# Performance work log

Hardware: AMD Instinct MI355X
Metric: run time of the kernel (lower is better)

Reference implementation:

```python
import jax, jax.numpy as jnp
import numpy as np
from jax import lax

NFEATS = 128
NMODES = 2
KH = KW = 3


def _conv_lstm_step(h, c, inp, W, b):
    """Standard ConvLSTMCell: conv over [inp, h] -> 4 gates -> c/h update.
    inp: (B, Cin, H, W); h, c: (B, nfeats, H, W); W: (4*nfeats, Cin+nfeats, 3, 3)."""
    z = lax.conv_general_dilated(
        jnp.concatenate([inp, h], axis=1), W,
        window_strides=(1, 1), padding='SAME',
        dimension_numbers=('NCHW', 'OIHW', 'NCHW'))
    z = z + b[None, :, None, None]
    i, f, o, g = jnp.split(z, 4, axis=1)
    c_next = jax.nn.sigmoid(f) * c + jax.nn.sigmoid(i) * jnp.tanh(g)
    h_next = jax.nn.sigmoid(o) * jnp.tanh(c_next)
    return h_next, c_next


def setup_inputs() -> dict:
    key = jax.random.key(0)
    ks = jax.random.split(key, 8)
    B, T, H, Wsp = 4, 8, 32, 32
    x1 = jax.random.normal(ks[0], (B, T, NFEATS, H, Wsp), dtype=jnp.float32)
    x2 = jax.random.normal(ks[1], (B, T, NFEATS, H, Wsp), dtype=jnp.float32)
    s = 0.02
    W1 = jax.random.normal(ks[2], (4 * NFEATS, NMODES * NFEATS + NFEATS, KH, KW), dtype=jnp.float32) * s
    b1 = jnp.zeros((4 * NFEATS,), dtype=jnp.float32)
    W2 = jax.random.normal(ks[3], (4 * NFEATS, 2 * NFEATS, KH, KW), dtype=jnp.float32) * s
    b2 = jnp.zeros((4 * NFEATS,), dtype=jnp.float32)
    W3 = jax.random.normal(ks[4], (4 * NFEATS, 2 * NFEATS, KH, KW), dtype=jnp.float32) * s
    b3 = jnp.zeros((4 * NFEATS,), dtype=jnp.float32)
    return {"x1": x1, "x2": x2, "W1": W1, "b1": b1, "W2": W2, "b2": b2, "W3": W3, "b3": b3}


def reference(x1, x2, W1, b1, W2, b2, W3, b3):
    # cat modalities on channel dim: (B, T, nmodes*nfeats, H, W)
    x = jnp.concatenate([x1, x2], axis=2)
    B, T, C, H, Wsp = x.shape
    zero = jnp.zeros((B, NFEATS, H, Wsp), dtype=x.dtype)
    carry0 = (zero, zero, zero, zero, zero, zero)  # h1,c1,h2,c2,h3,c3
    xs = jnp.moveaxis(x, 1, 0)  # (T, B, C, H, W)

    def step(carry, xt):
        h1, c1, h2, c2, h3, c3 = carry
        h1, c1 = _conv_lstm_step(h1, c1, xt, W1, b1)
        h2, c2 = _conv_lstm_step(h2, c2, h1, W2, b2)
        h3, c3 = _conv_lstm_step(h3, c3, h2, W3, b3)
        return (h1, c1, h2, c2, h3, c3), None

    (h1, c1, h2, c2, h3, c3), _ = lax.scan(step, carry0, xs)
    return h3
```

## Files before the change

### kernel.cpp

```cpp
#include <hip/hip_runtime.h>
#include <hip/hip_bf16.h>

typedef unsigned short u16;
typedef __attribute__((ext_vector_type(8))) short short8;
typedef __attribute__((ext_vector_type(4))) short short4v;
typedef __attribute__((ext_vector_type(4))) float floatx4;

__device__ __forceinline__ u16 f2bf(float x) {
  unsigned u = __float_as_uint(x);
  u += 0x7fffu + ((u >> 16) & 1u);
  return (u16)(u >> 16);
}
__device__ __forceinline__ float bf2f(u16 u) {
  return __uint_as_float(((unsigned)u) << 16);
}
__device__ __forceinline__ float sigm(float x) {
  return 1.0f / (1.0f + __expf(-x));
}


__global__ __launch_bounds__(256) void xsplit_kernel(
    const float* __restrict__ x1, const float* __restrict__ x2,
    u16* __restrict__ Xh, u16* __restrict__ Xl)
{
  __shared__ float lds[128][65];
  int bx  = blockIdx.x;
  int sel = bx >> 9;
  int rem = bx & 511;
  int bt  = rem >> 4;
  int pg  = rem & 15;
  int b = bt >> 3, t = bt & 7;
  int p0 = pg << 6;
  const float* src = (sel ? x2 : x1) + ((size_t)bt << 17);
  int tid = threadIdx.x;
  #pragma unroll
  for (int k2 = 0; k2 < 8; ++k2) {
    int idx = tid + (k2 << 8);
    int c = idx >> 4, p4 = (idx & 15) << 2;
    floatx4 v = *reinterpret_cast<const floatx4*>(src + ((size_t)c << 10) + p0 + p4);
    lds[c][p4] = v[0]; lds[c][p4 + 1] = v[1]; lds[c][p4 + 2] = v[2]; lds[c][p4 + 3] = v[3];
  }
  __syncthreads();
  int pl = tid >> 2;
  int cg = (tid & 3) << 5;
  size_t obase = (((size_t)((t * 4 + b) * 1024 + p0 + pl)) << 8) + (sel << 7) + cg;
  #pragma unroll
  for (int q = 0; q < 4; ++q) {
    short8 hv, lv;
    #pragma unroll
    for (int j = 0; j < 8; ++j) {
      float f = lds[cg + q * 8 + j][pl];
      u16 h = f2bf(f);
      hv[j] = (short)h;
      lv[j] = (short)f2bf(f - bf2f(h));
    }
    *reinterpret_cast<short8*>(Xh + obase + q * 8) = hv;
    *reinterpret_cast<short8*>(Xl + obase + q * 8) = lv;
  }
}

__global__ __launch_bounds__(256) void wsplit_kernel(
    const float* __restrict__ W, u16* __restrict__ Wh, u16* __restrict__ Wl, int CIN)
{
  int K = CIN * 9;
  int i = blockIdx.x * 256 + threadIdx.x;
  int np = i / K;
  int k = i - np * K;
  int e9 = k / CIN;
  int ci = k - e9 * CIN;
  int n = (np & 3) * 128 + (np >> 2);
  float v = W[((size_t)n * CIN + ci) * 9 + e9];
  size_t o = ((size_t)((np >> 4) * (K >> 3) + (k >> 3)) * 16 + (np & 15)) * 8 + (k & 7);
  u16 h = f2bf(v);
  Wh[o] = h;
  Wl[o] = f2bf(v - bf2f(h));
}

__global__ __launch_bounds__(256) void init_state(
    float* __restrict__ c1, float* __restrict__ c2, float* __restrict__ c3,
    u16* __restrict__ h1h, u16* __restrict__ h1l,
    u16* __restrict__ h2h, u16* __restrict__ h2l,
    u16* __restrict__ h3h, u16* __restrict__ h3l)
{
  int i = blockIdx.x * 256 + threadIdx.x;
  c1[i] = 0.f; c2[i] = 0.f; c3[i] = 0.f;
  h1h[i] = 0; h1l[i] = 0; h2h[i] = 0; h2l[i] = 0; h3h[i] = 0; h3l[i] = 0;
}

template<bool FUSE, int YR, int BPC>
__global__ __launch_bounds__(256, BPC) void conv_gemm(
    const u16* __restrict__ A1h, const u16* __restrict__ A1l, int CA,
    const u16* __restrict__ A2h, const u16* __restrict__ A2l, int CB,
    const u16* __restrict__ Wh, const u16* __restrict__ Wl,
    int WCIN, int wcoff, int WK, int MT,
    float* __restrict__ zout,
    const float* __restrict__ zx,
    const float* __restrict__ bias,
    float* __restrict__ c, u16* __restrict__ hh, u16* __restrict__ hl,
    float* __restrict__ hout)
{
  constexpr int PROWS = (YR + 2) * 34;
  constexpr int HALOB = PROWS * 128;
  constexpr int MF = 2 * YR;
  constexpr int RLD = (PROWS * 8 + 255) / 256;
  const int CIN = CA + CB;

  __shared__ __align__(16) char smem[2 * HALOB];

  int tid = threadIdx.x;
  int bx  = blockIdx.x;
  int nt = bx / MT;
  int mt = bx - nt * MT;
  int m0 = mt * (32 * YR);
  int slot = m0 >> 10;
  int pbase = m0 & 1023;
  int y0 = pbase >> 5;
  int n0 = nt * 128;

  int lane = tid & 63, wid = tid >> 6;
  int nh = wid & 1, kh = wid >> 1;
  int fr = lane & 15, kq = lane >> 4;
  const int WK8 = WK >> 3;
  const int g16b = (n0 >> 4) + nh * 4;

  floatx4 acc[MF][4];
  #pragma unroll
  for (int i2 = 0; i2 < MF; ++i2)
    #pragma unroll
    for (int j2 = 0; j2 < 4; ++j2)
      acc[i2][j2] = (floatx4)0.0f;

  short8 RH[RLD], RL[RLD];
  const int NC = CIN >> 6;

  auto ldA = [&](int cc) {
    const u16 *sh, *sl; int cbase, CH;
    if (cc < CA) { sh = A1h; sl = A1l; cbase = cc;      CH = CA; }
    else         { sh = A2h; sl = A2l; cbase = cc - CA; CH = CB; }
    #pragma unroll
    for (int r = 0; r < RLD; ++r) {
      int u = tid + 256 * r;
      if (u < PROWS * 8) {
        int prow = u >> 3, cq = u & 7;
        int hrow = prow / 34;
        int xcol = prow - hrow * 34;
        int y = y0 - 1 + hrow;
        int x = xcol - 1;
        bool valid = ((unsigned)y < 32u) & ((unsigned)x < 32u);
        short8 vh = (short8)0, vl = (short8)0;
        if (valid) {
          size_t ab = (size_t)(slot * 1024 + y * 32 + x) * CH + cbase + cq * 8;
          vh = *reinterpret_cast<const short8*>(sh + ab);
          vl = *reinterpret_cast<const short8*>(sl + ab);
        }
        RH[r] = vh; RL[r] = vl;
      }
    }
  };

  auto stA = [&]() {
    #pragma unroll
    for (int r = 0; r < RLD; ++r) {
      int u = tid + 256 * r;
      if (u < PROWS * 8) {
        int prow = u >> 3, cq = u & 7;
        int off = prow * 128 + (((cq ^ (prow & 7)) & 7) << 4);
        *reinterpret_cast<short8*>(smem + off)         = RH[r];
        *reinterpret_cast<short8*>(smem + HALOB + off) = RL[r];
      }
    }
  };

  auto computeChunk = [&](int cc) {
    const int u0 = kh ? 9 : 0;
    short8 Bch[4], Bcl[4];
    {
      int kb = wcoff + (u0 >> 1) * WCIN + cc + (u0 & 1) * 32 + kq * 8;
      #pragma unroll
      for (int nf = 0; nf < 4; ++nf) {
        size_t bo = ((size_t)((g16b + nf) * WK8 + (kb >> 3)) * 16 + fr) * 8;
        Bch[nf] = *reinterpret_cast<const short8*>(Wh + bo);
        Bcl[nf] = *reinterpret_cast<const short8*>(Wl + bo);
      }
    }
    #pragma unroll 1
    for (int ui = 0; ui < 9; ++ui) {
      int u = u0 + ui;
      int e9 = u >> 1, ks = u & 1;
      short8 Bnh_[4], Bnl_[4];
      if (ui < 8) {
        int un = u + 1;
        int kb = wcoff + (un >> 1) * WCIN + cc + (un & 1) * 32 + kq * 8;
        #pragma unroll
        for (int nf = 0; nf < 4; ++nf) {
          size_t bo = ((size_t)((g16b + nf) * WK8 + (kb >> 3)) * 16 + fr) * 8;
          Bnh_[nf] = *reinterpret_cast<const short8*>(Wh + bo);
          Bnl_[nf] = *reinterpret_cast<const short8*>(Wl + bo);
        }
      }
      int dy = e9 / 3 - 1;
      int dx = e9 - (e9 / 3) * 3 - 1;
      short8 Ah_[MF], Al_[MF];
      #pragma unroll
      for (int mf = 0; mf < MF; ++mf) {
        int ar = mf * 16 + fr;
        int prow = ((ar >> 5) + 1 + dy) * 34 + (ar & 31) + 1 + dx;
        int off = prow * 128 + ((((ks * 4 + kq) ^ (prow & 7)) & 7) << 4);
        Ah_[mf] = *reinterpret_cast<const short8*>(smem + off);
        Al_[mf] = *reinterpret_cast<const short8*>(smem + HALOB + off);
      }
      __builtin_amdgcn_s_setprio(1);
      #pragma unroll
      for (int mf = 0; mf < MF; ++mf)
        #pragma unroll
        for (int nf = 0; nf < 4; ++nf)
          acc[mf][nf] = __builtin_amdgcn_mfma_f32_16x16x32_bf16(Ah_[mf], Bch[nf], acc[mf][nf], 0, 0, 0);
      #pragma unroll
      for (int mf = 0; mf < MF; ++mf)
        #pragma unroll
        for (int nf = 0; nf < 4; ++nf)
          acc[mf][nf] = __builtin_amdgcn_mfma_f32_16x16x32_bf16(Ah_[mf], Bcl[nf], acc[mf][nf], 0, 0, 0);
      #pragma unroll
      for (int mf = 0; mf < MF; ++mf)
        #pragma unroll
        for (int nf = 0; nf < 4; ++nf)
          acc[mf][nf] = __builtin_amdgcn_mfma_f32_16x16x32_bf16(Al_[mf], Bch[nf], acc[mf][nf], 0, 0, 0);
      __builtin_amdgcn_s_setprio(0);
      if (ui < 8) {
        #pragma unroll
        for (int nf = 0; nf < 4; ++nf) { Bch[nf] = Bnh_[nf]; Bcl[nf] = Bnl_[nf]; }
      }
    }
  };

  ldA(0); stA();
  for (int q = 0; q < NC; ++q) {
    if (q + 1 < NC) ldA((q + 1) << 6);
    __syncthreads();
    computeChunk(q << 6);
    __syncthreads();
    if (q + 1 < NC) stA();
  }

  float (*tr)[68] = reinterpret_cast<float(*)[68]>(smem + nh * HALOB);
  if (kh == 0) {
    #pragma unroll
    for (int mf = 0; mf < MF; ++mf)
      #pragma unroll
      for (int nf = 0; nf < 4; ++nf)
        #pragma unroll
        for (int r = 0; r < 4; ++r)
          tr[mf * 16 + kq * 4 + r][nf * 16 + fr] = acc[mf][nf][r];
  }
  __syncthreads();
  if (kh == 1) {
    #pragma unroll
    for (int mf = 0; mf < MF; ++mf)
      #pragma unroll
      for (int nf = 0; nf < 4; ++nf)
        #pragma unroll
        for (int r = 0; r < 4; ++r)
          tr[mf * 16 + kq * 4 + r][nf * 16 + fr] += acc[mf][nf][r];
  }
  __syncthreads();

  int m  = (YR == 1) ? (lane & 31) : lane;
  int ol = (YR == 1) ? (lane >> 5) : 0;
  int ppix = pbase + m;
  size_t grow = (size_t)slot * 1024 + ppix;

  if (!FUSE) {
    size_t zrow = ((size_t)(m0 + m) << 9) + n0 + nh * 64 + kh * 32 + ol * 16;
    constexpr int NJ = (YR == 1) ? 4 : 8;
    #pragma unroll
    for (int j = 0; j < NJ; ++j) {
      floatx4 v = *reinterpret_cast<const floatx4*>(&tr[m][kh * 32 + ol * 16 + j * 4]);
      *reinterpret_cast<floatx4*>(zout + zrow + j * 4) = v;
    }
    return;
  }

  constexpr int NJ = (YR == 1) ? 4 : 8;
  int obc = kh * 8 + ol * 4;
  float cnv[NJ], hnv[NJ];
  #pragma unroll
  for (int j = 0; j < NJ; ++j) {
    int oc = obc + j;
    int ocg = nt * 32 + nh * 16 + oc;
    float zg[4];
    floatx4 tv = *reinterpret_cast<const floatx4*>(&tr[m][oc * 4]);
    if (zx) {
      floatx4 zv = *reinterpret_cast<const floatx4*>(zx + (grow << 9) + n0 + nh * 64 + oc * 4);
      #pragma unroll
      for (int g = 0; g < 4; ++g) zg[g] = tv[g] + zv[g] + bias[g * 128 + ocg];
    } else {
      #pragma unroll
      for (int g = 0; g < 4; ++g) zg[g] = tv[g] + bias[g * 128 + ocg];
    }
    size_t cidx = grow * 128 + ocg;
    float cvl = c[cidx];
    float cn = sigm(zg[1]) * cvl + sigm(zg[0]) * tanhf(zg[3]);
    float hn = sigm(zg[2]) * tanhf(cn);
    cnv[j] = cn; hnv[j] = hn;
    if (hout) hout[((size_t)slot * 128 + ocg) * 1024 + ppix] = hn;
  }
  size_t obase = grow * 128 + nt * 32 + nh * 16 + obc;
  if constexpr (YR == 1) {
    floatx4 cv; short4v hv, lv;
    #pragma unroll
    for (int j = 0; j < 4; ++j) {
      cv[j] = cnv[j];
      u16 hb = f2bf(hnv[j]);
      hv[j] = (short)hb;
      lv[j] = (short)f2bf(hnv[j] - bf2f(hb));
    }
    *reinterpret_cast<floatx4*>(c + obase) = cv;
    *reinterpret_cast<short4v*>(hh + obase) = hv;
    *reinterpret_cast<short4v*>(hl + obase) = lv;
  } else {
    floatx4 cv[2]; short8 hv, lv;
    #pragma unroll
    for (int j = 0; j < 8; ++j) {
      cv[j >> 2][j & 3] = cnv[j];
      u16 hb = f2bf(hnv[j]);
      hv[j] = (short)hb;
      lv[j] = (short)f2bf(hnv[j] - bf2f(hb));
    }
    *reinterpret_cast<floatx4*>(c + obase)     = cv[0];
    *reinterpret_cast<floatx4*>(c + obase + 4) = cv[1];
    *reinterpret_cast<short8*>(hh + obase) = hv;
    *reinterpret_cast<short8*>(hl + obase) = lv;
  }
}

extern "C" void kernel_launch(void* const* d_in, const int* in_sizes, int n_in,
                              void* d_out, int out_size, void* d_ws, size_t ws_size,
                              hipStream_t stream)
{
  const float* x1 = (const float*)d_in[0];
  const float* x2 = (const float*)d_in[1];
  const float* W1 = (const float*)d_in[2];
  const float* b1 = (const float*)d_in[3];
  const float* W2 = (const float*)d_in[4];
  const float* b2 = (const float*)d_in[5];
  const float* W3 = (const float*)d_in[6];
  const float* b3 = (const float*)d_in[7];
  float* out = (float*)d_out;

  char* ws = (char*)d_ws;
  size_t off = 0;
  auto alloc = [&](size_t bytes) {
    char* p = ws + off;
    off += (bytes + 255) & ~(size_t)255;
    return p;
  };
  u16*   Xh  = (u16*)  alloc(16777216);
  u16*   Xl  = (u16*)  alloc(16777216);
  u16*   W1h = (u16*)  alloc(3538944);
  u16*   W1l = (u16*)  alloc(3538944);
  u16*   W2h = (u16*)  alloc(2359296);
  u16*   W2l = (u16*)  alloc(2359296);
  u16*   W3h = (u16*)  alloc(2359296);
  u16*   W3l = (u16*)  alloc(2359296);
  u16*   hb_[12];
  for (int i = 0; i < 12; ++i) hb_[i] = (u16*)alloc(1048576);
  float* c1  = (float*)alloc(2097152);
  float* c2  = (float*)alloc(2097152);
  float* c3  = (float*)alloc(2097152);
  float* zx  = (float*)alloc(67108864);
  if (off > ws_size) return;

  u16 **h1h = &hb_[0], **h1l = &hb_[2], **h2h = &hb_[4], **h2l = &hb_[6],
      **h3h = &hb_[8], **h3l = &hb_[10];

  xsplit_kernel<<<1024, 256, 0, stream>>>(x1, x2, Xh, Xl);
  wsplit_kernel<<<6912, 256, 0, stream>>>(W1, W1h, W1l, 384);
  wsplit_kernel<<<4608, 256, 0, stream>>>(W2, W2h, W2l, 256);
  wsplit_kernel<<<4608, 256, 0, stream>>>(W3, W3h, W3l, 256);
  init_state<<<2048, 256, 0, stream>>>(c1, c2, c3,
      hb_[0], hb_[2], hb_[4], hb_[6], hb_[8], hb_[10]);

  conv_gemm<false, 2, 3><<<2048, 256, 0, stream>>>(
      Xh, Xl, 256, nullptr, nullptr, 0, W1h, W1l, 384, 0, 3456, 512,
      zx, nullptr, nullptr, nullptr, nullptr, nullptr, nullptr);

  for (int t = 0; t < 8; ++t) {
    int pi = t & 1, po = pi ^ 1;
    const float* zxt = zx + (size_t)t * 2097152;
    conv_gemm<true, 1, 2><<<512, 256, 0, stream>>>(
        h1h[pi], h1l[pi], 128, nullptr, nullptr, 0, W1h, W1l, 384, 256, 3456, 128,
        nullptr, zxt, b1, c1, h1h[po], h1l[po], nullptr);
    conv_gemm<true, 1, 2><<<512, 256, 0, stream>>>(
        h1h[po], h1l[po], 128, h2h[pi], h2l[pi], 128, W2h, W2l, 256, 0, 2304, 128,
        nullptr, nullptr, b2, c2, h2h[po], h2l[po], nullptr);
    conv_gemm<true, 1, 2><<<512, 256, 0, stream>>>(
        h2h[po], h2l[po], 128, h3h[pi], h3l[pi], 128, W3h, W3l, 256, 0, 2304, 128,
        nullptr, nullptr, b3, c3, h3h[po], h3l[po], (t == 7) ? out : nullptr);
  }
}
```

Before: 1.205 ms.

## Deepen weight prefetch pipeline, fully unroll tap loop, and remap block indices

The 9-step tap loop is now fully unrolled with a configurable prefetch depth for the weight fragments (depth 2 for the recurrent launches), so the global loads of B are issued further ahead of the MFMAs that use them. Block indices are remapped so that consecutive blocks interleave the four N tiles over pairs of M tiles, aiming to improve L2 reuse of weights and activations. The input-projection launch drops from 3 to 2 blocks per CU in its launch bounds. Full unrolling and the deeper prefetch raise register pressure and code size, which could lower occupancy. The fixed index mapping also hardcodes four N tiles.

```diff
diff --git a/kernel.cpp b/kernel.cpp
--- a/kernel.cpp
+++ b/kernel.cpp
@@ -87,12 +87,12 @@
   h1h[i] = 0; h1l[i] = 0; h2h[i] = 0; h2l[i] = 0; h3h[i] = 0; h3l[i] = 0;
 }
 
-template<bool FUSE, int YR, int BPC>
+template<bool FUSE, int YR, int BPC, int DEPTH>
 __global__ __launch_bounds__(256, BPC) void conv_gemm(
     const u16* __restrict__ A1h, const u16* __restrict__ A1l, int CA,
     const u16* __restrict__ A2h, const u16* __restrict__ A2l, int CB,
     const u16* __restrict__ Wh, const u16* __restrict__ Wl,
-    int WCIN, int wcoff, int WK, int MT,
+    int WCIN, int wcoff, int WK,
     float* __restrict__ zout,
     const float* __restrict__ zx,
     const float* __restrict__ bias,
@@ -109,8 +109,8 @@
 
   int tid = threadIdx.x;
   int bx  = blockIdx.x;
-  int nt = bx / MT;
-  int mt = bx - nt * MT;
+  int nt = (bx & 7) >> 1;
+  int mt = ((bx >> 3) << 1) | (bx & 1);
   int m0 = mt * (32 * YR);
   int slot = m0 >> 10;
   int pbase = m0 & 1023;
@@ -173,31 +173,31 @@
 
   auto computeChunk = [&](int cc) {
     const int u0 = kh ? 9 : 0;
-    short8 Bch[4], Bcl[4];
-    {
-      int kb = wcoff + (u0 >> 1) * WCIN + cc + (u0 & 1) * 32 + kq * 8;
+    short8 Bh_[9 + DEPTH][4], Bl_[9 + DEPTH][4];
+    #pragma unroll
+    for (int d = 0; d < DEPTH; ++d) {
+      int kb = wcoff + ((u0 + d) >> 1) * WCIN + cc + ((u0 + d) & 1) * 32 + kq * 8;
       #pragma unroll
       for (int nf = 0; nf < 4; ++nf) {
         size_t bo = ((size_t)((g16b + nf) * WK8 + (kb >> 3)) * 16 + fr) * 8;
-        Bch[nf] = *reinterpret_cast<const short8*>(Wh + bo);
-        Bcl[nf] = *reinterpret_cast<const short8*>(Wl + bo);
-      }
-    }
-    #pragma unroll 1
+        Bh_[d][nf] = *reinterpret_cast<const short8*>(Wh + bo);
+        Bl_[d][nf] = *reinterpret_cast<const short8*>(Wl + bo);
+      }
+    }
+    #pragma unroll
     for (int ui = 0; ui < 9; ++ui) {
+      if (ui + DEPTH < 9) {
+        int un = u0 + ui + DEPTH;
+        int kb = wcoff + (un >> 1) * WCIN + cc + (un & 1) * 32 + kq * 8;
+        #pragma unroll
+        for (int nf = 0; nf < 4; ++nf) {
+          size_t bo = ((size_t)((g16b + nf) * WK8 + (kb >> 3)) * 16 + fr) * 8;
+          Bh_[ui + DEPTH][nf] = *reinterpret_cast<const short8*>(Wh + bo);
+          Bl_[ui + DEPTH][nf] = *reinterpret_cast<const short8*>(Wl + bo);
+        }
+      }
       int u = u0 + ui;
       int e9 = u >> 1, ks = u & 1;
-      short8 Bnh_[4], Bnl_[4];
-      if (ui < 8) {
-        int un = u + 1;
-        int kb = wcoff + (un >> 1) * WCIN + cc + (un & 1) * 32 + kq * 8;
-        #pragma unroll
-        for (int nf = 0; nf < 4; ++nf) {
-          size_t bo = ((size_t)((g16b + nf) * WK8 + (kb >> 3)) * 16 + fr) * 8;
-          Bnh_[nf] = *reinterpret_cast<const short8*>(Wh + bo);
-          Bnl_[nf] = *reinterpret_cast<const short8*>(Wl + bo);
-        }
-      }
       int dy = e9 / 3 - 1;
       int dx = e9 - (e9 / 3) * 3 - 1;
       short8 Ah_[MF], Al_[MF];
@@ -214,22 +214,18 @@
       for (int mf = 0; mf < MF; ++mf)
         #pragma unroll
         for (int nf = 0; nf < 4; ++nf)
-          acc[mf][nf] = __builtin_amdgcn_mfma_f32_16x16x32_bf16(Ah_[mf], Bch[nf], acc[mf][nf], 0, 0, 0);
+          acc[mf][nf] = __builtin_amdgcn_mfma_f32_16x16x32_bf16(Ah_[mf], Bh_[ui][nf], acc[mf][nf], 0, 0, 0);
       #pragma unroll
       for (int mf = 0; mf < MF; ++mf)
         #pragma unroll
         for (int nf = 0; nf < 4; ++nf)
-          acc[mf][nf] = __builtin_amdgcn_mfma_f32_16x16x32_bf16(Ah_[mf], Bcl[nf], acc[mf][nf], 0, 0, 0);
+          acc[mf][nf] = __builtin_amdgcn_mfma_f32_16x16x32_bf16(Ah_[mf], Bl_[ui][nf], acc[mf][nf], 0, 0, 0);
       #pragma unroll
       for (int mf = 0; mf < MF; ++mf)
         #pragma unroll
         for (int nf = 0; nf < 4; ++nf)
-          acc[mf][nf] = __builtin_amdgcn_mfma_f32_16x16x32_bf16(Al_[mf], Bch[nf], acc[mf][nf], 0, 0, 0);
+          acc[mf][nf] = __builtin_amdgcn_mfma_f32_16x16x32_bf16(Al_[mf], Bh_[ui][nf], acc[mf][nf], 0, 0, 0);
       __builtin_amdgcn_s_setprio(0);
-      if (ui < 8) {
-        #pragma unroll
-        for (int nf = 0; nf < 4; ++nf) { Bch[nf] = Bnh_[nf]; Bcl[nf] = Bnl_[nf]; }
-      }
     }
   };
 
@@ -380,21 +376,21 @@
   init_state<<<2048, 256, 0, stream>>>(c1, c2, c3,
       hb_[0], hb_[2], hb_[4], hb_[6], hb_[8], hb_[10]);
 
-  conv_gemm<false, 2, 3><<<2048, 256, 0, stream>>>(
-      Xh, Xl, 256, nullptr, nullptr, 0, W1h, W1l, 384, 0, 3456, 512,
+  conv_gemm<false, 2, 2, 1><<<2048, 256, 0, stream>>>(
+      Xh, Xl, 256, nullptr, nullptr, 0, W1h, W1l, 384, 0, 3456,
       zx, nullptr, nullptr, nullptr, nullptr, nullptr, nullptr);
 
   for (int t = 0; t < 8; ++t) {
     int pi = t & 1, po = pi ^ 1;
     const float* zxt = zx + (size_t)t * 2097152;
-    conv_gemm<true, 1, 2><<<512, 256, 0, stream>>>(
-        h1h[pi], h1l[pi], 128, nullptr, nullptr, 0, W1h, W1l, 384, 256, 3456, 128,
+    conv_gemm<true, 1, 2, 2><<<512, 256, 0, stream>>>(
+        h1h[pi], h1l[pi], 128, nullptr, nullptr, 0, W1h, W1l, 384, 256, 3456,
         nullptr, zxt, b1, c1, h1h[po], h1l[po], nullptr);
-    conv_gemm<true, 1, 2><<<512, 256, 0, stream>>>(
-        h1h[po], h1l[po], 128, h2h[pi], h2l[pi], 128, W2h, W2l, 256, 0, 2304, 128,
+    conv_gemm<true, 1, 2, 2><<<512, 256, 0, stream>>>(
+        h1h[po], h1l[po], 128, h2h[pi], h2l[pi], 128, W2h, W2l, 256, 0, 2304,
         nullptr, nullptr, b2, c2, h2h[po], h2l[po], nullptr);
-    conv_gemm<true, 1, 2><<<512, 256, 0, stream>>>(
-        h2h[po], h2l[po], 128, h3h[pi], h3l[pi], 128, W3h, W3l, 256, 0, 2304, 128,
+    conv_gemm<true, 1, 2, 2><<<512, 256, 0, stream>>>(
+        h2h[po], h2l[po], 128, h3h[pi], h3l[pi], 128, W3h, W3l, 256, 0, 2304,
         nullptr, nullptr, b3, c3, h3h[po], h3l[po], (t == 7) ? out : nullptr);
   }
 }
```

Result: faster. 1.048 ms (-13.0%).
